# Performance work log

Hardware: AMD Instinct MI355X
Metric: run time of the kernel (lower is better)

Reference implementation:

```python
import jax, jax.numpy as jnp
import numpy as np

P, L = 4, 2                      # meta-paths, sub-layers
N_NODES, N_EDGES = 100000, 1600000
E_TABLE = 200000                 # global edge-feature table rows
D_IN = D_OUT = 128
D_META, NREG = 64, 50000
SCALE = np.float32(1.0 / np.sqrt(D_OUT))


def setup_inputs() -> dict:
    key = jax.random.key(0)
    ks = jax.random.split(key, 8)
    E = jax.random.normal(ks[0], (E_TABLE, D_IN), jnp.float32)
    metapath_emb = jax.random.normal(ks[1], (P, D_META), jnp.float32)
    W_root = jax.random.normal(ks[2], (P, L, D_IN, D_OUT), jnp.float32) * 0.05
    W_rel = jax.random.normal(ks[3], (P, L, D_IN, D_OUT), jnp.float32) * 0.05
    b = jnp.zeros((P, L, D_OUT), jnp.float32)
    Wq = jax.random.normal(ks[4], (D_META, D_OUT), jnp.float32) * 0.05
    bq = jnp.zeros((D_OUT,), jnp.float32)
    edge_index = jax.random.randint(ks[5], (P, 2, N_EDGES), 0, N_NODES, dtype=jnp.int64)
    eids = jax.random.randint(ks[6], (P, N_NODES), 0, E_TABLE, dtype=jnp.int64)
    return dict(E=E, metapath_emb=metapath_emb, W_root=W_root, W_rel=W_rel, b=b,
                Wq=Wq, bq=bq, edge_index=edge_index, eids=eids)


def _rgcn(x, src, dst, Wr, Wm, bias):
    # PyG RGCNConv, single relation, mean aggregation:
    # h_i = mean_{j->i}(x_j @ Wm) + x_i @ Wr + bias
    msg = x[src] @ Wm                                           # [E, d_out]
    agg = jax.ops.segment_sum(msg, dst, num_segments=N_NODES)   # [N, d_out]
    cnt = jax.ops.segment_sum(jnp.ones((src.shape[0], 1), x.dtype), dst,
                              num_segments=N_NODES)
    return agg / jnp.maximum(cnt, 1.0) + x @ Wr + bias


def reference(E, metapath_emb, W_root, W_rel, b, Wq, bq, edge_index, eids):
    sems = []
    for i in range(P):                      # small fixed loop over meta-paths
        src, dst = edge_index[i, 0], edge_index[i, 1]
        x = E[eids[i]]                      # gather edge features, [N, d_in]
        for j in range(L):
            x = jax.nn.relu(_rgcn(x, src, dst, W_root[i, j], W_rel[i, j], b[i, j]))
        sems.append(x[:NREG])
    emb = jnp.stack(sems, axis=1)           # [NREG, P, d_out]
    query = metapath_emb @ Wq + bq          # [P, d_out]
    # bmm + diagonal extraction == per-(n,p) dot product
    scores = jnp.einsum('pd,npd->np', query, emb) * SCALE
    w = jax.nn.softmax(scores, axis=1)      # softmax over meta-paths
    return jnp.sum(w[:, :, None] * emb, axis=1)   # [NREG, d_out]
```

## Files before the change

kernel.cpp:

```cpp
#include <hip/hip_runtime.h>

#define N_NODES 100000
#define N_EDGES 1600000
#define E_TBL   200000
#define D       128
#define NREG    50000
#define P_MP    4
#define L_SUB   2
#define D_META  64
#define SCALE_F 0.08838834764831845f

#define BKT_SHIFT 9
#define BKT_NODES 512
#define NBKT      196
#define CSB       128
#define EPB       (N_EDGES / CSB)
#define P2N       (NBKT * CSB)
#define P2B       (P2N / 256)

typedef __attribute__((ext_vector_type(8))) short bf16x8;
typedef __attribute__((ext_vector_type(4))) float f32x4;


__device__ __forceinline__ float bf2f_lo(unsigned int u) {
    union { unsigned int i; float f; } v;
    v.i = u << 16;
    return v.f;
}
__device__ __forceinline__ float bf2f_hi(unsigned int u) {
    union { unsigned int i; float f; } v;
    v.i = u & 0xffff0000u;
    return v.f;
}
__device__ __forceinline__ unsigned int f2bf(float f) {
    union { float f; unsigned int i; } v;
    v.f = f;
    return (v.i + 0x7fffu + ((v.i >> 16) & 1u)) >> 16;
}


__global__ __launch_bounds__(256) void p1_bhist(const int* __restrict__ edge_index,
                                                int* __restrict__ tbl) {
    __shared__ int h[NBKT];
    int p = blockIdx.y, b = blockIdx.x, t = threadIdx.x;
    const int* dst = edge_index + ((size_t)p * 2 + 1) * N_EDGES;
    if (t < NBKT) h[t] = 0;
    __syncthreads();
    int e0 = b * EPB;
    for (int e = e0 + t; e < e0 + EPB; e += 256)
        atomicAdd(&h[dst[e] >> BKT_SHIFT], 1);
    __syncthreads();
    if (t < NBKT) tbl[(size_t)p * P2N + t * CSB + b] = h[t];
}


__global__ __launch_bounds__(1024) void p2_scan(const int* __restrict__ tbl,
                                                int* __restrict__ tblx,
                                                int* __restrict__ offs) {
    __shared__ int ts[1024];
    int p = blockIdx.x, t = threadIdx.x;
    const int* tp = tbl + (size_t)p * P2N;
    int* xp = tblx + (size_t)p * P2N;
    int v[25];
    int base = t * 25;
    int sum = 0;
#pragma unroll
    for (int i = 0; i < 25; ++i) {
        int idx = base + i;
        int val = (idx < P2N) ? tp[idx] : 0;
        v[i] = val;
        sum += val;
    }
    ts[t] = sum;
    __syncthreads();
    for (int o = 1; o < 1024; o <<= 1) {
        int u = (t >= o) ? ts[t - o] : 0;
        __syncthreads();
        ts[t] += u;
        __syncthreads();
    }
    int run = ts[t] - sum;
#pragma unroll
    for (int i = 0; i < 25; ++i) {
        int idx = base + i;
        if (idx < P2N) xp[idx] = run;
        run += v[i];
    }
    if (t == 0) offs[(size_t)p * (N_NODES + 1) + N_NODES] = N_EDGES;
}


__global__ __launch_bounds__(256) void p3_coarse(const int* __restrict__ edge_index,
                                                 const int* __restrict__ tblx,
                                                 uint2* __restrict__ pairs) {
    __shared__ int lcur[NBKT];
    int p = blockIdx.y, b = blockIdx.x, t = threadIdx.x;
    const int* src = edge_index + ((size_t)p * 2 + 0) * N_EDGES;
    const int* dst = edge_index + ((size_t)p * 2 + 1) * N_EDGES;
    const int* txp = tblx + (size_t)p * P2N;
    uint2* pp = pairs + (size_t)p * N_EDGES;
    if (t < NBKT) lcur[t] = txp[t * CSB + b];
    __syncthreads();
    int e0 = b * EPB;
    for (int e = e0 + t; e < e0 + EPB; e += 256) {
        int d = dst[e], s0 = src[e];
        int pos = atomicAdd(&lcur[d >> BKT_SHIFT], 1);
        pp[pos] = make_uint2((unsigned)s0, (unsigned)d);
    }
}


__global__ __launch_bounds__(256) void p4_fine(const uint2* __restrict__ pairs,
                                               const int* __restrict__ tblx,
                                               int* __restrict__ offs,
                                               int* __restrict__ ssrc) {
    __shared__ int lhist[BKT_NODES];
    __shared__ int lcur[BKT_NODES];
    __shared__ int pr[256];
    int p = blockIdx.y, b = blockIdx.x, t = threadIdx.x;
    const uint2* pp = pairs + (size_t)p * N_EDGES;
    const int* txp = tblx + (size_t)p * P2N;
    int* offp = offs + (size_t)p * (N_NODES + 1);
    int* sp = ssrc + (size_t)p * N_EDGES;
    int nbase = b << BKT_SHIFT;
    int e0 = txp[b * CSB];
    int e1 = (b + 1 < NBKT) ? txp[(b + 1) * CSB] : N_EDGES;
    lhist[t] = 0;
    lhist[t + 256] = 0;
    __syncthreads();
    for (int e = e0 + t; e < e1; e += 256)
        atomicAdd(&lhist[pp[e].y - nbase], 1);
    __syncthreads();
    int c0 = lhist[2 * t], c1 = lhist[2 * t + 1];
    int ps = c0 + c1;
    pr[t] = ps;
    __syncthreads();
    for (int o = 1; o < 256; o <<= 1) {
        int u = (t >= o) ? pr[t - o] : 0;
        __syncthreads();
        pr[t] += u;
        __syncthreads();
    }
    int ex = e0 + pr[t] - ps;
    lcur[2 * t] = ex;
    lcur[2 * t + 1] = ex + c0;
    int n0 = nbase + 2 * t;
    if (n0 < N_NODES)     offp[n0] = ex;
    if (n0 + 1 < N_NODES) offp[n0 + 1] = ex + c0;
    __syncthreads();
    for (int e = e0 + t; e < e1; e += 256) {
        uint2 q = pp[e];
        int pos = atomicAdd(&lcur[q.y - nbase], 1);
        sp[pos] = (int)q.x;
    }
}


__global__ __launch_bounds__(256) void k_gather(const float* __restrict__ Etab,
                                                const int* __restrict__ eids,
                                                unsigned short* __restrict__ x0) {
    int p = blockIdx.y;
    int i = blockIdx.x * 256 + threadIdx.x;
    int n = i >> 4, g = i & 15;
    if (n >= N_NODES) return;
    int r = eids[(size_t)p * N_NODES + n];
    const float4* srcp = (const float4*)(Etab + (size_t)r * D + g * 8);
    float4 a = srcp[0], b = srcp[1];
    uint4 o;
    o.x = f2bf(a.x) | (f2bf(a.y) << 16);
    o.y = f2bf(a.z) | (f2bf(a.w) << 16);
    o.z = f2bf(b.x) | (f2bf(b.y) << 16);
    o.w = f2bf(b.z) | (f2bf(b.w) << 16);
    *(uint4*)(x0 + ((size_t)p * N_NODES + n) * D + g * 8) = o;
}


__global__ __launch_bounds__(256) void k_spmm(const unsigned short* __restrict__ x,
                                              const int* __restrict__ offs,
                                              const int* __restrict__ ssrc,
                                              unsigned short* __restrict__ sout, int rows) {
    int p = blockIdx.y;
    int lane = threadIdx.x & 63;
    int wv = __builtin_amdgcn_readfirstlane((blockIdx.x * 256 + (int)threadIdx.x) >> 6);
    if (wv >= rows) return;
    const int* offp = offs + (size_t)p * (N_NODES + 1);
    const int* ep = ssrc + (size_t)p * N_EDGES;
    const unsigned int* xb = (const unsigned int*)x + (size_t)p * N_NODES * 64;
    int e0 = __builtin_amdgcn_readfirstlane(offp[wv]);
    int e1 = __builtin_amdgcn_readfirstlane(offp[wv + 1]);
    float ax = 0.f, ay = 0.f;

    int e = e0;
    while (e < e1) {
        int m = min(64, e1 - e);
        int idx = (lane < m) ? ep[e + lane] : 0;
        int j = 0;
        for (; j + 8 <= m; j += 8) {
            int s0 = __builtin_amdgcn_readlane(idx, j + 0);
            int s1 = __builtin_amdgcn_readlane(idx, j + 1);
            int s2 = __builtin_amdgcn_readlane(idx, j + 2);
            int s3 = __builtin_amdgcn_readlane(idx, j + 3);
            int s4 = __builtin_amdgcn_readlane(idx, j + 4);
            int s5 = __builtin_amdgcn_readlane(idx, j + 5);
            int s6 = __builtin_amdgcn_readlane(idx, j + 6);
            int s7 = __builtin_amdgcn_readlane(idx, j + 7);
            unsigned int v0 = xb[(size_t)s0 * 64 + lane];
            unsigned int v1 = xb[(size_t)s1 * 64 + lane];
            unsigned int v2 = xb[(size_t)s2 * 64 + lane];
            unsigned int v3 = xb[(size_t)s3 * 64 + lane];
            unsigned int v4 = xb[(size_t)s4 * 64 + lane];
            unsigned int v5 = xb[(size_t)s5 * 64 + lane];
            unsigned int v6 = xb[(size_t)s6 * 64 + lane];
            unsigned int v7 = xb[(size_t)s7 * 64 + lane];
            ax += bf2f_lo(v0) + bf2f_lo(v1) + bf2f_lo(v2) + bf2f_lo(v3)
                + bf2f_lo(v4) + bf2f_lo(v5) + bf2f_lo(v6) + bf2f_lo(v7);
            ay += bf2f_hi(v0) + bf2f_hi(v1) + bf2f_hi(v2) + bf2f_hi(v3)
                + bf2f_hi(v4) + bf2f_hi(v5) + bf2f_hi(v6) + bf2f_hi(v7);
        }
        if (j + 4 <= m) {
            int s0 = __builtin_amdgcn_readlane(idx, j + 0);
            int s1 = __builtin_amdgcn_readlane(idx, j + 1);
            int s2 = __builtin_amdgcn_readlane(idx, j + 2);
            int s3 = __builtin_amdgcn_readlane(idx, j + 3);
            unsigned int v0 = xb[(size_t)s0 * 64 + lane];
            unsigned int v1 = xb[(size_t)s1 * 64 + lane];
            unsigned int v2 = xb[(size_t)s2 * 64 + lane];
            unsigned int v3 = xb[(size_t)s3 * 64 + lane];
            ax += bf2f_lo(v0) + bf2f_lo(v1) + bf2f_lo(v2) + bf2f_lo(v3);
            ay += bf2f_hi(v0) + bf2f_hi(v1) + bf2f_hi(v2) + bf2f_hi(v3);
            j += 4;
        }
        for (; j < m; ++j) {
            int sj = __builtin_amdgcn_readlane(idx, j);
            unsigned int v = xb[(size_t)sj * 64 + lane];
            ax += bf2f_lo(v);
            ay += bf2f_hi(v);
        }
        e += m;
    }

    int deg = e1 - e0;
    float inv = 1.0f / (float)(deg > 0 ? deg : 1);
    unsigned int o = f2bf(ax * inv) | (f2bf(ay * inv) << 16);
    ((unsigned int*)sout)[((size_t)p * rows + wv) * 64 + lane] = o;
}


__global__ __launch_bounds__(256) void k_wswz(const float* __restrict__ Wroot,
                                              const float* __restrict__ Wrel,
                                              unsigned short* __restrict__ wswz) {
    int gid = blockIdx.x * blockDim.x + threadIdx.x;
    if (gid >= 16 * 4 * 8 * 64) return;
    int lane = gid & 63;
    int t = (gid >> 6) & 7;
    int c = (gid >> 9) & 3;
    int mat = gid >> 11;
    int which = mat & 1;
    int pl = mat >> 1;
    const float* W = (which == 0 ? Wrel : Wroot) + (size_t)pl * D * D;
    int k0 = c * 32 + (lane >> 4) * 8;
    int n = t * 16 + (lane & 15);
    unsigned short o[8];
#pragma unroll
    for (int j = 0; j < 8; ++j) o[j] = (unsigned short)f2bf(W[(size_t)(k0 + j) * D + n]);
    *(uint4*)(wswz + ((size_t)((mat * 4 + c) * 8 + t) * 64 + lane) * 8) = *(uint4*)o;
}


template <bool OUT_BF16>
__global__ __launch_bounds__(256) void k_mgemm(const unsigned short* __restrict__ sb,
                                               const unsigned short* __restrict__ xbase,
                                               const unsigned short* __restrict__ wswz,
                                               const float* __restrict__ bvec,
                                               void* __restrict__ outv,
                                               int M, int layer, int out_stride) {
    int p = blockIdx.y;
    int widl = (blockIdx.x * 256 + (int)threadIdx.x) >> 6;
    int lane = threadIdx.x & 63;
    int row0 = widl << 4;
    if (row0 >= M) return;
    const unsigned short* s = sb + (size_t)p * M * D;
    const unsigned short* x = xbase + (size_t)p * N_NODES * D;
    const unsigned short* wm = wswz + (size_t)((p * L_SUB + layer) * 2 + 0) * D * D;
    const unsigned short* wr = wswz + (size_t)((p * L_SUB + layer) * 2 + 1) * D * D;
    const float* bias = bvec + (size_t)(p * L_SUB + layer) * D;

    int arow = row0 + (lane & 15);
    int asub = (lane >> 4) * 8;

    union U { uint4 u; bf16x8 v; };
    f32x4 acc[8];
#pragma unroll
    for (int t = 0; t < 8; ++t) acc[t] = (f32x4){0.f, 0.f, 0.f, 0.f};

#pragma unroll
    for (int c = 0; c < 4; ++c) {
        U as, ax;
        as.u = *(const uint4*)(s + (size_t)arow * D + c * 32 + asub);
        ax.u = *(const uint4*)(x + (size_t)arow * D + c * 32 + asub);
#pragma unroll
        for (int t = 0; t < 8; ++t) {
            U bm, br;
            bm.u = *(const uint4*)(wm + ((size_t)((c * 8 + t) * 64) + lane) * 8);
            br.u = *(const uint4*)(wr + ((size_t)((c * 8 + t) * 64) + lane) * 8);
            acc[t] = __builtin_amdgcn_mfma_f32_16x16x32_bf16(as.v, bm.v, acc[t], 0, 0, 0);
            acc[t] = __builtin_amdgcn_mfma_f32_16x16x32_bf16(ax.v, br.v, acc[t], 0, 0, 0);
        }
    }

    int colb = lane & 15;
    int rq = (lane >> 4) * 4;
#pragma unroll
    for (int t = 0; t < 8; ++t) {
        int col = t * 16 + colb;
        float bv = bias[col];
#pragma unroll
        for (int r = 0; r < 4; ++r) {
            float v = fmaxf(acc[t][r] + bv, 0.f);
            size_t off = ((size_t)p * out_stride + row0 + rq + r) * D + col;
            if (OUT_BF16) ((unsigned short*)outv)[off] = (unsigned short)f2bf(v);
            else          ((float*)outv)[off] = v;
        }
    }
}


__global__ void k_query(const float* __restrict__ meta, const float* __restrict__ Wq,
                        const float* __restrict__ bq, float* __restrict__ query) {
    int t = blockIdx.x * blockDim.x + threadIdx.x;
    if (t < P_MP * D) {
        int p = t >> 7, c = t & 127;
        float acc = bq[c];
        for (int k = 0; k < D_META; ++k) acc += meta[p * D_META + k] * Wq[k * D + c];
        query[t] = acc;
    }
}


__global__ __launch_bounds__(256) void k_final(const float* __restrict__ emb,
                                               const float* __restrict__ query,
                                               float* __restrict__ out) {
    int wv = (blockIdx.x * blockDim.x + threadIdx.x) >> 6;
    int lane = threadIdx.x & 63;
    if (wv >= NREG) return;
    float2 e[4];
    float sc[4];
#pragma unroll
    for (int p = 0; p < 4; ++p) {
        e[p] = *(const float2*)(emb + ((size_t)p * NREG + wv) * D + lane * 2);
        float2 q = *(const float2*)(query + p * D + lane * 2);
        float d = e[p].x * q.x + e[p].y * q.y;
#pragma unroll
        for (int o = 32; o > 0; o >>= 1) d += __shfl_xor(d, o, 64);
        sc[p] = d * SCALE_F;
    }
    float mx = fmaxf(fmaxf(sc[0], sc[1]), fmaxf(sc[2], sc[3]));
    float w[4], sum = 0.f;
#pragma unroll
    for (int p = 0; p < 4; ++p) { w[p] = __expf(sc[p] - mx); sum += w[p]; }
    float inv = 1.f / sum;
    float ox = 0.f, oy = 0.f;
#pragma unroll
    for (int p = 0; p < 4; ++p) { ox += w[p] * inv * e[p].x; oy += w[p] * inv * e[p].y; }
    float2 o; o.x = ox; o.y = oy;
    *(float2*)(out + (size_t)wv * D + lane * 2) = o;
}


extern "C" void kernel_launch(void* const* d_in, const int* in_sizes, int n_in,
                              void* d_out, int out_size, void* d_ws, size_t ws_size,
                              hipStream_t stream) {
    const float* Etab  = (const float*)d_in[0];
    const float* meta  = (const float*)d_in[1];
    const float* Wroot = (const float*)d_in[2];
    const float* Wrel  = (const float*)d_in[3];
    const float* bvec  = (const float*)d_in[4];
    const float* Wq    = (const float*)d_in[5];
    const float* bq    = (const float*)d_in[6];
    const int* edge_index = (const int*)d_in[7];
    const int* eids       = (const int*)d_in[8];
    float* out = (float*)d_out;

    char* w = (char*)d_ws;
    char* regionA = w;                           w += (size_t)P_MP * N_NODES * D * 2;
    unsigned short* h1   = (unsigned short*)w;   w += (size_t)P_MP * N_NODES * D * 2;
    unsigned short* sbuf = (unsigned short*)w;   w += (size_t)P_MP * N_NODES * D * 2;
    int* ssrc = (int*)w;                         w += (size_t)P_MP * N_EDGES * 4;
    int* offs = (int*)w;                         w += (size_t)P_MP * (N_NODES + 1) * 4 + 240;
    int* tbl  = (int*)w;                         w += (size_t)P_MP * P2N * 4;
    int* tblx = (int*)w;                         w += (size_t)P_MP * P2N * 4;
    unsigned short* wswz = (unsigned short*)w;   w += (size_t)16 * D * D * 2;
    float* query = (float*)w;                    w += 4096;

    uint2* pairs       = (uint2*)regionA;
    unsigned short* x0 = (unsigned short*)regionA;
    float* emb         = (float*)regionA;

    k_wswz<<<128, 256, 0, stream>>>(Wroot, Wrel, wswz);
    k_query<<<2, 256, 0, stream>>>(meta, Wq, bq, query);

    p1_bhist<<<dim3(CSB, P_MP), 256, 0, stream>>>(edge_index, tbl);
    p2_scan<<<dim3(P_MP), 1024, 0, stream>>>(tbl, tblx, offs);
    p3_coarse<<<dim3(CSB, P_MP), 256, 0, stream>>>(edge_index, tblx, pairs);
    p4_fine<<<dim3(NBKT, P_MP), 256, 0, stream>>>(pairs, tblx, offs, ssrc);

    k_gather<<<dim3(N_NODES * 16 / 256, P_MP), 256, 0, stream>>>(Etab, eids, x0);

    k_spmm<<<dim3(N_NODES / 4, P_MP), 256, 0, stream>>>(x0, offs, ssrc, sbuf, N_NODES);
    k_mgemm<true><<<dim3((N_NODES / 16 + 3) / 4, P_MP), 256, 0, stream>>>(
        sbuf, x0, wswz, bvec, h1, N_NODES, 0, N_NODES);

    k_spmm<<<dim3(NREG / 4, P_MP), 256, 0, stream>>>(h1, offs, ssrc, sbuf, NREG);
    k_mgemm<false><<<dim3((NREG / 16 + 3) / 4, P_MP), 256, 0, stream>>>(
        sbuf, h1, wswz, bvec, emb, NREG, 1, NREG);

    k_final<<<(NREG * 64) / 256, 256, 0, stream>>>(emb, query, out);
}
```

Baseline: 907.1 us.

## Process four edges per wave in SpMM with 16-byte row loads

The SpMM gather kernel now splits each 64-lane wave into four 16-lane quarters. Each quarter fetches a different neighbor row using 16-byte loads, and source indices are distributed with ds_bpermute instead of scalar readlane. Partial sums are combined across quarters with xor shuffles before 16 lanes write the output row. This aims to raise the number of memory requests in flight and cut per-edge instruction overhead, at the cost of LDS permute traffic, a cross-lane reduction, and idle lanes in the remainder handling.

```diff
diff --git a/kernel.cpp b/kernel.cpp
--- a/kernel.cpp
+++ b/kernel.cpp
@@ -20,6 +20,7 @@
 
 typedef __attribute__((ext_vector_type(8))) short bf16x8;
 typedef __attribute__((ext_vector_type(4))) float f32x4;
+typedef __attribute__((ext_vector_type(2))) float f32x2;
 
 
 __device__ __forceinline__ float bf2f_lo(unsigned int u) {
@@ -52,7 +53,6 @@
     __syncthreads();
     if (t < NBKT) tbl[(size_t)p * P2N + t * CSB + b] = h[t];
 }
-
 
 __global__ __launch_bounds__(1024) void p2_scan(const int* __restrict__ tbl,
                                                 int* __restrict__ tblx,
@@ -89,7 +89,6 @@
     if (t == 0) offs[(size_t)p * (N_NODES + 1) + N_NODES] = N_EDGES;
 }
 
-
 __global__ __launch_bounds__(256) void p3_coarse(const int* __restrict__ edge_index,
                                                  const int* __restrict__ tblx,
                                                  uint2* __restrict__ pairs) {
@@ -108,7 +107,6 @@
         pp[pos] = make_uint2((unsigned)s0, (unsigned)d);
     }
 }
-
 
 __global__ __launch_bounds__(256) void p4_fine(const uint2* __restrict__ pairs,
                                                const int* __restrict__ tblx,
@@ -175,6 +173,14 @@
 }
 
 
+__device__ __forceinline__ void acc4(uint4 r, f32x2& a01, f32x2& a23, f32x2& a45, f32x2& a67) {
+    f32x2 t;
+    t.x = bf2f_lo(r.x); t.y = bf2f_hi(r.x); a01 += t;
+    t.x = bf2f_lo(r.y); t.y = bf2f_hi(r.y); a23 += t;
+    t.x = bf2f_lo(r.z); t.y = bf2f_hi(r.z); a45 += t;
+    t.x = bf2f_lo(r.w); t.y = bf2f_hi(r.w); a67 += t;
+}
+
 __global__ __launch_bounds__(256) void k_spmm(const unsigned short* __restrict__ x,
                                               const int* __restrict__ offs,
                                               const int* __restrict__ ssrc,
@@ -185,64 +191,70 @@
     if (wv >= rows) return;
     const int* offp = offs + (size_t)p * (N_NODES + 1);
     const int* ep = ssrc + (size_t)p * N_EDGES;
-    const unsigned int* xb = (const unsigned int*)x + (size_t)p * N_NODES * 64;
+    const char* xbb = (const char*)x + (size_t)p * N_NODES * 256;
     int e0 = __builtin_amdgcn_readfirstlane(offp[wv]);
     int e1 = __builtin_amdgcn_readfirstlane(offp[wv + 1]);
-    float ax = 0.f, ay = 0.f;
+
+    int qb   = (lane >> 4) << 2;
+    unsigned lo16 = (unsigned)(lane & 15) << 4;
+
+    f32x2 a01 = {0.f, 0.f}, a23 = {0.f, 0.f}, a45 = {0.f, 0.f}, a67 = {0.f, 0.f};
 
     int e = e0;
     while (e < e1) {
         int m = min(64, e1 - e);
-        int idx = (lane < m) ? ep[e + lane] : 0;
-        int j = 0;
-        for (; j + 8 <= m; j += 8) {
-            int s0 = __builtin_amdgcn_readlane(idx, j + 0);
-            int s1 = __builtin_amdgcn_readlane(idx, j + 1);
-            int s2 = __builtin_amdgcn_readlane(idx, j + 2);
-            int s3 = __builtin_amdgcn_readlane(idx, j + 3);
-            int s4 = __builtin_amdgcn_readlane(idx, j + 4);
-            int s5 = __builtin_amdgcn_readlane(idx, j + 5);
-            int s6 = __builtin_amdgcn_readlane(idx, j + 6);
-            int s7 = __builtin_amdgcn_readlane(idx, j + 7);
-            unsigned int v0 = xb[(size_t)s0 * 64 + lane];
-            unsigned int v1 = xb[(size_t)s1 * 64 + lane];
-            unsigned int v2 = xb[(size_t)s2 * 64 + lane];
-            unsigned int v3 = xb[(size_t)s3 * 64 + lane];
-            unsigned int v4 = xb[(size_t)s4 * 64 + lane];
-            unsigned int v5 = xb[(size_t)s5 * 64 + lane];
-            unsigned int v6 = xb[(size_t)s6 * 64 + lane];
-            unsigned int v7 = xb[(size_t)s7 * 64 + lane];
-            ax += bf2f_lo(v0) + bf2f_lo(v1) + bf2f_lo(v2) + bf2f_lo(v3)
-                + bf2f_lo(v4) + bf2f_lo(v5) + bf2f_lo(v6) + bf2f_lo(v7);
-            ay += bf2f_hi(v0) + bf2f_hi(v1) + bf2f_hi(v2) + bf2f_hi(v3)
-                + bf2f_hi(v4) + bf2f_hi(v5) + bf2f_hi(v6) + bf2f_hi(v7);
+        int v = (lane < m) ? ep[e + lane] : 0;
+        int m4 = m >> 2;
+        int k = 0;
+        for (; k + 4 <= m4; k += 4) {
+            int i0 = __builtin_amdgcn_ds_bpermute(qb + ((k + 0) << 4), v);
+            int i1 = __builtin_amdgcn_ds_bpermute(qb + ((k + 1) << 4), v);
+            int i2 = __builtin_amdgcn_ds_bpermute(qb + ((k + 2) << 4), v);
+            int i3 = __builtin_amdgcn_ds_bpermute(qb + ((k + 3) << 4), v);
+            uint4 r0 = *(const uint4*)(xbb + ((((unsigned)i0) << 8) | lo16));
+            uint4 r1 = *(const uint4*)(xbb + ((((unsigned)i1) << 8) | lo16));
+            uint4 r2 = *(const uint4*)(xbb + ((((unsigned)i2) << 8) | lo16));
+            uint4 r3 = *(const uint4*)(xbb + ((((unsigned)i3) << 8) | lo16));
+            acc4(r0, a01, a23, a45, a67);
+            acc4(r1, a01, a23, a45, a67);
+            acc4(r2, a01, a23, a45, a67);
+            acc4(r3, a01, a23, a45, a67);
         }
-        if (j + 4 <= m) {
-            int s0 = __builtin_amdgcn_readlane(idx, j + 0);
-            int s1 = __builtin_amdgcn_readlane(idx, j + 1);
-            int s2 = __builtin_amdgcn_readlane(idx, j + 2);
-            int s3 = __builtin_amdgcn_readlane(idx, j + 3);
-            unsigned int v0 = xb[(size_t)s0 * 64 + lane];
-            unsigned int v1 = xb[(size_t)s1 * 64 + lane];
-            unsigned int v2 = xb[(size_t)s2 * 64 + lane];
-            unsigned int v3 = xb[(size_t)s3 * 64 + lane];
-            ax += bf2f_lo(v0) + bf2f_lo(v1) + bf2f_lo(v2) + bf2f_lo(v3);
-            ay += bf2f_hi(v0) + bf2f_hi(v1) + bf2f_hi(v2) + bf2f_hi(v3);
-            j += 4;
+        for (; k < m4; ++k) {
+            int i0 = __builtin_amdgcn_ds_bpermute(qb + (k << 4), v);
+            uint4 r0 = *(const uint4*)(xbb + ((((unsigned)i0) << 8) | lo16));
+            acc4(r0, a01, a23, a45, a67);
         }
-        for (; j < m; ++j) {
-            int sj = __builtin_amdgcn_readlane(idx, j);
-            unsigned int v = xb[(size_t)sj * 64 + lane];
-            ax += bf2f_lo(v);
-            ay += bf2f_hi(v);
+        int rem = m & 3;
+        if (rem) {
+            int iv = __builtin_amdgcn_ds_bpermute(qb + (m4 << 4), v);
+            if ((lane >> 4) < rem) {
+                uint4 r = *(const uint4*)(xbb + ((((unsigned)iv) << 8) | lo16));
+                acc4(r, a01, a23, a45, a67);
+            }
         }
         e += m;
     }
 
+#pragma unroll
+    for (int o = 32; o >= 16; o >>= 1) {
+        f32x2 t;
+        t.x = __shfl_xor(a01.x, o, 64); t.y = __shfl_xor(a01.y, o, 64); a01 += t;
+        t.x = __shfl_xor(a23.x, o, 64); t.y = __shfl_xor(a23.y, o, 64); a23 += t;
+        t.x = __shfl_xor(a45.x, o, 64); t.y = __shfl_xor(a45.y, o, 64); a45 += t;
+        t.x = __shfl_xor(a67.x, o, 64); t.y = __shfl_xor(a67.y, o, 64); a67 += t;
+    }
+
     int deg = e1 - e0;
     float inv = 1.0f / (float)(deg > 0 ? deg : 1);
-    unsigned int o = f2bf(ax * inv) | (f2bf(ay * inv) << 16);
-    ((unsigned int*)sout)[((size_t)p * rows + wv) * 64 + lane] = o;
+    if (lane < 16) {
+        uint4 o;
+        o.x = f2bf(a01.x * inv) | (f2bf(a01.y * inv) << 16);
+        o.y = f2bf(a23.x * inv) | (f2bf(a23.y * inv) << 16);
+        o.z = f2bf(a45.x * inv) | (f2bf(a45.y * inv) << 16);
+        o.w = f2bf(a67.x * inv) | (f2bf(a67.y * inv) << 16);
+        *(uint4*)((char*)sout + ((size_t)p * rows + wv) * 256 + lo16) = o;
+    }
 }
 
 
```

Result: no change. 903.0 us (-0.4%).

## Slice node features into 16-column panels and map one thread per destination in SpMM

Applied to the files above, without the earlier changes.

Node features are now stored as 8 slices of 16 bf16 columns (a 32-byte row per slice), written that way by gather and by the first-layer GEMM epilogue and read that way by the GEMM A-operand loads. SpMM changes from one wavefront per destination row (readlane broadcast of source indices, each lane reading one 4-byte word) to one thread per destination per slice. Each thread reads 32 contiguous bytes per neighbor and keeps 16 accumulators. The aim is to make each slice's working set small enough to stay cache-resident and to drop the per-row wave overhead, at the cost of uncoalesced per-thread index loads and load imbalance across threads with different degrees.

```diff
diff --git a/kernel.cpp b/kernel.cpp
--- a/kernel.cpp
+++ b/kernel.cpp
@@ -16,10 +16,11 @@
 #define CSB       128
 #define EPB       (N_EDGES / CSB)
 #define P2N       (NBKT * CSB)
-#define P2B       (P2N / 256)
 
 typedef __attribute__((ext_vector_type(8))) short bf16x8;
 typedef __attribute__((ext_vector_type(4))) float f32x4;
+typedef __attribute__((ext_vector_type(2))) float f32x2;
+typedef __attribute__((ext_vector_type(4))) unsigned int u32x4;
 
 
 __device__ __forceinline__ float bf2f_lo(unsigned int u) {
@@ -52,7 +53,6 @@
     __syncthreads();
     if (t < NBKT) tbl[(size_t)p * P2N + t * CSB + b] = h[t];
 }
-
 
 __global__ __launch_bounds__(1024) void p2_scan(const int* __restrict__ tbl,
                                                 int* __restrict__ tblx,
@@ -89,7 +89,6 @@
     if (t == 0) offs[(size_t)p * (N_NODES + 1) + N_NODES] = N_EDGES;
 }
 
-
 __global__ __launch_bounds__(256) void p3_coarse(const int* __restrict__ edge_index,
                                                  const int* __restrict__ tblx,
                                                  uint2* __restrict__ pairs) {
@@ -108,7 +107,6 @@
         pp[pos] = make_uint2((unsigned)s0, (unsigned)d);
     }
 }
-
 
 __global__ __launch_bounds__(256) void p4_fine(const uint2* __restrict__ pairs,
                                                const int* __restrict__ tblx,
@@ -171,78 +169,68 @@
     o.y = f2bf(a.z) | (f2bf(a.w) << 16);
     o.z = f2bf(b.x) | (f2bf(b.y) << 16);
     o.w = f2bf(b.z) | (f2bf(b.w) << 16);
-    *(uint4*)(x0 + ((size_t)p * N_NODES + n) * D + g * 8) = o;
+    int s = g >> 1, h = g & 1;
+    *(uint4*)(x0 + ((size_t)(p * 8 + s) * N_NODES + n) * 16 + h * 8) = o;
 }
 
 
 __global__ __launch_bounds__(256) void k_spmm(const unsigned short* __restrict__ x,
                                               const int* __restrict__ offs,
                                               const int* __restrict__ ssrc,
-                                              unsigned short* __restrict__ sout, int rows) {
+                                              unsigned short* __restrict__ sout,
+                                              int rows) {
     int p = blockIdx.y;
-    int lane = threadIdx.x & 63;
-    int wv = __builtin_amdgcn_readfirstlane((blockIdx.x * 256 + (int)threadIdx.x) >> 6);
-    if (wv >= rows) return;
+    int slice = blockIdx.x & 7;
+    int blk = blockIdx.x >> 3;
+    int dst = blk * 256 + (int)threadIdx.x;
+    if (dst >= rows) return;
     const int* offp = offs + (size_t)p * (N_NODES + 1);
     const int* ep = ssrc + (size_t)p * N_EDGES;
-    const unsigned int* xb = (const unsigned int*)x + (size_t)p * N_NODES * 64;
-    int e0 = __builtin_amdgcn_readfirstlane(offp[wv]);
-    int e1 = __builtin_amdgcn_readfirstlane(offp[wv + 1]);
-    float ax = 0.f, ay = 0.f;
+    const unsigned short* xs = x + (size_t)(p * 8 + slice) * N_NODES * 16;
+    int e0 = offp[dst], e1 = offp[dst + 1];
+
+    f32x2 a[8];
+#pragma unroll
+    for (int k = 0; k < 8; ++k) a[k] = (f32x2){0.f, 0.f};
+
+#define ACCU(u, k) { f32x2 t; t.x = bf2f_lo(u); t.y = bf2f_hi(u); a[k] += t; }
+#define ACC8(ra, rb) { ACCU(ra.x, 0) ACCU(ra.y, 1) ACCU(ra.z, 2) ACCU(ra.w, 3) \
+                       ACCU(rb.x, 4) ACCU(rb.y, 5) ACCU(rb.z, 6) ACCU(rb.w, 7) }
 
     int e = e0;
-    while (e < e1) {
-        int m = min(64, e1 - e);
-        int idx = (lane < m) ? ep[e + lane] : 0;
-        int j = 0;
-        for (; j + 8 <= m; j += 8) {
-            int s0 = __builtin_amdgcn_readlane(idx, j + 0);
-            int s1 = __builtin_amdgcn_readlane(idx, j + 1);
-            int s2 = __builtin_amdgcn_readlane(idx, j + 2);
-            int s3 = __builtin_amdgcn_readlane(idx, j + 3);
-            int s4 = __builtin_amdgcn_readlane(idx, j + 4);
-            int s5 = __builtin_amdgcn_readlane(idx, j + 5);
-            int s6 = __builtin_amdgcn_readlane(idx, j + 6);
-            int s7 = __builtin_amdgcn_readlane(idx, j + 7);
-            unsigned int v0 = xb[(size_t)s0 * 64 + lane];
-            unsigned int v1 = xb[(size_t)s1 * 64 + lane];
-            unsigned int v2 = xb[(size_t)s2 * 64 + lane];
-            unsigned int v3 = xb[(size_t)s3 * 64 + lane];
-            unsigned int v4 = xb[(size_t)s4 * 64 + lane];
-            unsigned int v5 = xb[(size_t)s5 * 64 + lane];
-            unsigned int v6 = xb[(size_t)s6 * 64 + lane];
-            unsigned int v7 = xb[(size_t)s7 * 64 + lane];
-            ax += bf2f_lo(v0) + bf2f_lo(v1) + bf2f_lo(v2) + bf2f_lo(v3)
-                + bf2f_lo(v4) + bf2f_lo(v5) + bf2f_lo(v6) + bf2f_lo(v7);
-            ay += bf2f_hi(v0) + bf2f_hi(v1) + bf2f_hi(v2) + bf2f_hi(v3)
-                + bf2f_hi(v4) + bf2f_hi(v5) + bf2f_hi(v6) + bf2f_hi(v7);
-        }
-        if (j + 4 <= m) {
-            int s0 = __builtin_amdgcn_readlane(idx, j + 0);
-            int s1 = __builtin_amdgcn_readlane(idx, j + 1);
-            int s2 = __builtin_amdgcn_readlane(idx, j + 2);
-            int s3 = __builtin_amdgcn_readlane(idx, j + 3);
-            unsigned int v0 = xb[(size_t)s0 * 64 + lane];
-            unsigned int v1 = xb[(size_t)s1 * 64 + lane];
-            unsigned int v2 = xb[(size_t)s2 * 64 + lane];
-            unsigned int v3 = xb[(size_t)s3 * 64 + lane];
-            ax += bf2f_lo(v0) + bf2f_lo(v1) + bf2f_lo(v2) + bf2f_lo(v3);
-            ay += bf2f_hi(v0) + bf2f_hi(v1) + bf2f_hi(v2) + bf2f_hi(v3);
-            j += 4;
-        }
-        for (; j < m; ++j) {
-            int sj = __builtin_amdgcn_readlane(idx, j);
-            unsigned int v = xb[(size_t)sj * 64 + lane];
-            ax += bf2f_lo(v);
-            ay += bf2f_hi(v);
-        }
-        e += m;
-    }
+    for (; e + 2 <= e1; e += 2) {
+        int s0 = __builtin_nontemporal_load(ep + e);
+        int s1 = __builtin_nontemporal_load(ep + e + 1);
+        const uint4* r0p = (const uint4*)(xs + (size_t)s0 * 16);
+        const uint4* r1p = (const uint4*)(xs + (size_t)s1 * 16);
+        uint4 r0a = r0p[0], r0b = r0p[1];
+        uint4 r1a = r1p[0], r1b = r1p[1];
+        ACC8(r0a, r0b)
+        ACC8(r1a, r1b)
+    }
+    if (e < e1) {
+        int s0 = __builtin_nontemporal_load(ep + e);
+        const uint4* r0p = (const uint4*)(xs + (size_t)s0 * 16);
+        uint4 r0a = r0p[0], r0b = r0p[1];
+        ACC8(r0a, r0b)
+    }
+#undef ACC8
+#undef ACCU
 
     int deg = e1 - e0;
     float inv = 1.0f / (float)(deg > 0 ? deg : 1);
-    unsigned int o = f2bf(ax * inv) | (f2bf(ay * inv) << 16);
-    ((unsigned int*)sout)[((size_t)p * rows + wv) * 64 + lane] = o;
+    u32x4 o0, o1;
+    o0.x = f2bf(a[0].x * inv) | (f2bf(a[0].y * inv) << 16);
+    o0.y = f2bf(a[1].x * inv) | (f2bf(a[1].y * inv) << 16);
+    o0.z = f2bf(a[2].x * inv) | (f2bf(a[2].y * inv) << 16);
+    o0.w = f2bf(a[3].x * inv) | (f2bf(a[3].y * inv) << 16);
+    o1.x = f2bf(a[4].x * inv) | (f2bf(a[4].y * inv) << 16);
+    o1.y = f2bf(a[5].x * inv) | (f2bf(a[5].y * inv) << 16);
+    o1.z = f2bf(a[6].x * inv) | (f2bf(a[6].y * inv) << 16);
+    o1.w = f2bf(a[7].x * inv) | (f2bf(a[7].y * inv) << 16);
+    unsigned short* op = sout + ((size_t)(p * 8 + slice) * rows + dst) * 16;
+    __builtin_nontemporal_store(o0, (u32x4*)op);
+    __builtin_nontemporal_store(o1, (u32x4*)(op + 8));
 }
 
 
@@ -269,24 +257,22 @@
 
 template <bool OUT_BF16>
 __global__ __launch_bounds__(256) void k_mgemm(const unsigned short* __restrict__ sb,
-                                               const unsigned short* __restrict__ xbase,
+                                               const unsigned short* __restrict__ xb,
                                                const unsigned short* __restrict__ wswz,
                                                const float* __restrict__ bvec,
                                                void* __restrict__ outv,
                                                int M, int layer, int out_stride) {
     int p = blockIdx.y;
     int widl = (blockIdx.x * 256 + (int)threadIdx.x) >> 6;
-    int lane = threadIdx.x & 63;
+    int lane = (int)threadIdx.x & 63;
     int row0 = widl << 4;
     if (row0 >= M) return;
-    const unsigned short* s = sb + (size_t)p * M * D;
-    const unsigned short* x = xbase + (size_t)p * N_NODES * D;
     const unsigned short* wm = wswz + (size_t)((p * L_SUB + layer) * 2 + 0) * D * D;
     const unsigned short* wr = wswz + (size_t)((p * L_SUB + layer) * 2 + 1) * D * D;
     const float* bias = bvec + (size_t)(p * L_SUB + layer) * D;
 
     int arow = row0 + (lane & 15);
-    int asub = (lane >> 4) * 8;
+    int q = lane >> 4, h = q & 1, qh = q >> 1;
 
     union U { uint4 u; bf16x8 v; };
     f32x4 acc[8];
@@ -295,9 +281,10 @@
 
 #pragma unroll
     for (int c = 0; c < 4; ++c) {
+        int s2 = c * 2 + qh;
         U as, ax;
-        as.u = *(const uint4*)(s + (size_t)arow * D + c * 32 + asub);
-        ax.u = *(const uint4*)(x + (size_t)arow * D + c * 32 + asub);
+        as.u = *(const uint4*)(sb + ((size_t)(p * 8 + s2) * M + arow) * 16 + h * 8);
+        ax.u = *(const uint4*)(xb + ((size_t)(p * 8 + s2) * N_NODES + arow) * 16 + h * 8);
 #pragma unroll
         for (int t = 0; t < 8; ++t) {
             U bm, br;
@@ -317,9 +304,13 @@
 #pragma unroll
         for (int r = 0; r < 4; ++r) {
             float v = fmaxf(acc[t][r] + bv, 0.f);
-            size_t off = ((size_t)p * out_stride + row0 + rq + r) * D + col;
-            if (OUT_BF16) ((unsigned short*)outv)[off] = (unsigned short)f2bf(v);
-            else          ((float*)outv)[off] = v;
+            int row = row0 + rq + r;
+            if (OUT_BF16) {
+                ((unsigned short*)outv)[((size_t)(p * 8 + t) * out_stride + row) * 16 + colb] =
+                    (unsigned short)f2bf(v);
+            } else {
+                ((float*)outv)[((size_t)p * out_stride + row) * D + col] = v;
+            }
         }
     }
 }
@@ -406,13 +397,19 @@
 
     k_gather<<<dim3(N_NODES * 16 / 256, P_MP), 256, 0, stream>>>(Etab, eids, x0);
 
-    k_spmm<<<dim3(N_NODES / 4, P_MP), 256, 0, stream>>>(x0, offs, ssrc, sbuf, N_NODES);
-    k_mgemm<true><<<dim3((N_NODES / 16 + 3) / 4, P_MP), 256, 0, stream>>>(
-        sbuf, x0, wswz, bvec, h1, N_NODES, 0, N_NODES);
-
-    k_spmm<<<dim3(NREG / 4, P_MP), 256, 0, stream>>>(h1, offs, ssrc, sbuf, NREG);
-    k_mgemm<false><<<dim3((NREG / 16 + 3) / 4, P_MP), 256, 0, stream>>>(
-        sbuf, h1, wswz, bvec, emb, NREG, 1, NREG);
+    {
+        int nb = (N_NODES + 255) / 256;
+        k_spmm<<<dim3(8 * nb, P_MP), 256, 0, stream>>>(x0, offs, ssrc, sbuf, N_NODES);
+        k_mgemm<true><<<dim3((N_NODES / 16 + 3) / 4, P_MP), 256, 0, stream>>>(
+            sbuf, x0, wswz, bvec, h1, N_NODES, 0, N_NODES);
+    }
+
+    {
+        int nb = (NREG + 255) / 256;
+        k_spmm<<<dim3(8 * nb, P_MP), 256, 0, stream>>>(h1, offs, ssrc, sbuf, NREG);
+        k_mgemm<false><<<dim3((NREG / 16 + 3) / 4, P_MP), 256, 0, stream>>>(
+            sbuf, h1, wswz, bvec, emb, NREG, 1, NREG);
+    }
 
     k_final<<<(NREG * 64) / 256, 256, 0, stream>>>(emb, query, out);
 }
```

New measurement: 1.484 ms. 1.64x slower.
